# Optimization experiments

Hardware: AMD Instinct MI355X
Metric: run time of the kernel (lower is better)

The kernel has to match this reference:

```python
import jax, jax.numpy as jnp
import numpy as np

D_MODEL = 1024
D_HEAD = 64

def setup_inputs() -> dict:
    key = jax.random.key(0)
    kx, kk, kq, kv = jax.random.split(key, 4)
    s = D_MODEL ** -0.5
    return {
        "x": jax.random.normal(kx, (4, 4096, D_MODEL), dtype=jnp.float32),
        "Wk": jax.random.normal(kk, (D_MODEL, D_HEAD), dtype=jnp.float32) * s,
        "Wq": jax.random.normal(kq, (D_MODEL, D_HEAD), dtype=jnp.float32) * s,
        "Wv": jax.random.normal(kv, (D_MODEL, D_HEAD), dtype=jnp.float32) * s,
    }

def reference(x, Wk, Wq, Wv):
    # x: [B, T, d_model]; Wk/Wq/Wv: [d_model, d_head]
    B, T, _ = x.shape
    d_head = Wk.shape[1]
    k = x @ Wk  # [B, T, d_head]
    q = x @ Wq
    v = x @ Wv
    scores = jnp.einsum("btd,bsd->bts", q, k) * (d_head ** -0.5)  # [B, T, T]
    causal = jnp.tril(jnp.ones((T, T), dtype=bool))
    scores = jnp.where(causal, scores, -jnp.inf)
    weights = jax.nn.softmax(scores, axis=-1)
    return jnp.einsum("bts,bsd->btd", weights, v)
```

## Files before the change

kernel.cpp:

```cpp
#include <hip/hip_runtime.h>

typedef __attribute__((ext_vector_type(8))) short bf16x8;
typedef __attribute__((ext_vector_type(4))) float f32x4;

#define DI __device__ __forceinline__

DI unsigned short f2bf(float f) {
    unsigned int u = __builtin_bit_cast(unsigned int, f);
    u += 0x7fff + ((u >> 16) & 1);
    return (unsigned short)(u >> 16);
}

DI unsigned int cvtpk(float lo, float hi) {
    unsigned int r;
    asm("v_cvt_pk_bf16_f32 %0, %1, %2" : "=v"(r) : "v"(lo), "v"(hi));
    return r;
}

DI void gl_lds16(const void* g, void* l) {
    __builtin_amdgcn_global_load_lds(
        (const __attribute__((address_space(1))) unsigned int*)g,
        (__attribute__((address_space(3))) unsigned int*)l, 16, 0, 0);
}

#define WAITCNT(n) asm volatile("s_waitcnt vmcnt(" #n ")" ::: "memory")

__global__ __launch_bounds__(256) void wt_kernel(
    const float* __restrict__ Wk, const float* __restrict__ Wq,
    const float* __restrict__ Wv, unsigned short* __restrict__ Wt)
{
    __shared__ float ws[64][65];
    const int m = blockIdx.x >> 4, kc = blockIdx.x & 15;
    const float* W = (m == 0) ? Wq : (m == 1) ? Wk : Wv;
    const float scale = (m == 0) ? 0.18033688011112042f : 1.0f;
    const int tid = threadIdx.x;
    #pragma unroll
    for (int r = 0; r < 16; ++r) {
        int idx = r * 256 + tid;
        ws[idx >> 6][idx & 63] = W[(kc * 64 + (idx >> 6)) * 64 + (idx & 63)] * scale;
    }
    __syncthreads();
    const int c = tid >> 2, k4 = (tid & 3) * 16;
    bf16x8 o0, o1;
    #pragma unroll
    for (int j = 0; j < 8; ++j) o0[j] = (short)f2bf(ws[k4 + j][c]);
    #pragma unroll
    for (int j = 0; j < 8; ++j) o1[j] = (short)f2bf(ws[k4 + 8 + j][c]);
    unsigned short* dst = Wt + ((size_t)m * 64 + c) * 1024 + kc * 64 + k4;
    *(bf16x8*)dst = o0;
    *(bf16x8*)(dst + 8) = o1;
}

__global__ __launch_bounds__(256) void proj_kernel(
    const float* __restrict__ x, const unsigned short* __restrict__ Wt,
    unsigned short* __restrict__ qw, unsigned short* __restrict__ kw,
    unsigned short* __restrict__ vT)
{
    __shared__ char LDSx[3][8192];
    __shared__ char LDSb[3][6144];

    const int tid = threadIdx.x;
    const int w = tid >> 6, l = tid & 63;
    const int xr = l & 15, lg = l >> 4;
    const int rb = blockIdx.x & 255, ch = blockIdx.x >> 8;
    const int row0 = rb * 64;

    const char* xsrc = (const char*)x + (size_t)row0 * 4096;
    const char* Wtb = (const char*)Wt;

    const int xrow_l = l >> 3, xcb = (l & 7) * 16;
    const int brow_l = l >> 2, bcb = (l & 3) * 16;

    auto stage = [&](int nb, int s) {
        #pragma unroll
        for (int c = 0; c < 4; ++c) {
            const int ci = w + 4 * c;
            if (ci < 8) {
                const int row = ci * 8 + xrow_l;
                const int sw = (row & 7) << 4;
                gl_lds16(xsrc + (size_t)row * 4096 + (size_t)s * 128 + (xcb ^ sw),
                         LDSx[nb] + ci * 1024);
            } else if (ci < 14) {
                const int c8 = ci - 8;
                const int r = c8 * 16 + brow_l;
                const int sw = ((r >> 1) & 3) << 4;
                const int wtrow = (r >> 5) * 64 + ch * 32 + (r & 31);
                gl_lds16(Wtb + (size_t)wtrow * 2048 + (size_t)s * 64 + (bcb ^ sw),
                         LDSb[nb] + c8 * 1024);
            }
        }
    };

    f32x4 acc[3][2];
    #pragma unroll
    for (int m = 0; m < 3; ++m)
        #pragma unroll
        for (int tt = 0; tt < 2; ++tt) { f32x4 z = {0.f,0.f,0.f,0.f}; acc[m][tt] = z; }

    const int Rw = w * 16 + xr;
    const int swx = (Rw & 7) << 4;

    auto compute = [&](int pb) {
        float4 va = *(const float4*)(LDSx[pb] + Rw * 128 + ((32 * lg) ^ swx));
        float4 vb = *(const float4*)(LDSx[pb] + Rw * 128 + ((32 * lg + 16) ^ swx));
        bf16x8 a;
        a[0] = (short)f2bf(va.x); a[1] = (short)f2bf(va.y);
        a[2] = (short)f2bf(va.z); a[3] = (short)f2bf(va.w);
        a[4] = (short)f2bf(vb.x); a[5] = (short)f2bf(vb.y);
        a[6] = (short)f2bf(vb.z); a[7] = (short)f2bf(vb.w);
        __builtin_amdgcn_s_setprio(1);
        #pragma unroll
        for (int m = 0; m < 3; ++m)
            #pragma unroll
            for (int tt = 0; tt < 2; ++tt) {
                const int rB = m * 32 + tt * 16 + xr;
                bf16x8 bfr = *(const bf16x8*)(LDSb[pb] + rB * 64 +
                                ((16 * lg) ^ (((rB >> 1) & 3) << 4)));
                acc[m][tt] = __builtin_amdgcn_mfma_f32_16x16x32_bf16(a, bfr, acc[m][tt], 0, 0, 0);
            }
        __builtin_amdgcn_s_setprio(0);
    };

    stage(0, 0); stage(1, 1);

    int cb = 0, nb = 2;
    for (int s = 0; s < 32; ++s) {
        if (s == 31) { WAITCNT(0); }
        else if (w < 2) { WAITCNT(4); }
        else { WAITCNT(3); }
        __builtin_amdgcn_sched_barrier(0);
        __builtin_amdgcn_s_barrier();
        if (s + 2 < 32) stage(nb, s + 2);
        compute(cb);
        cb = (cb == 2) ? 0 : cb + 1;
        nb = (nb == 2) ? 0 : nb + 1;
    }

    const int bb = row0 >> 12;
    #pragma unroll
    for (int tt = 0; tt < 2; ++tt) {
        const int col = ch * 32 + tt * 16 + xr;
        unsigned short pv4[4];
        #pragma unroll
        for (int i = 0; i < 4; ++i) {
            const int grow = row0 + w * 16 + 4 * lg + i;
            qw[(size_t)grow * 64 + col] = f2bf(acc[0][tt][i]);
            kw[(size_t)grow * 64 + col] = f2bf(acc[1][tt][i]);
            pv4[i] = f2bf(acc[2][tt][i]);
        }
        const int lr0 = (row0 & 4095) + w * 16 + 4 * lg;
        *(uint2*)&vT[((size_t)bb * 64 + col) * 4096 + lr0] = *(const uint2*)pv4;
    }
}

__global__ __launch_bounds__(256) void attn_kernel(
    const unsigned short* __restrict__ qw, const unsigned short* __restrict__ kw,
    const unsigned short* __restrict__ vT,
    unsigned short* __restrict__ POb, float* __restrict__ Pl)
{
    __shared__ __align__(16) unsigned short Kb[2][4096];
    __shared__ __align__(16) unsigned short Vb[2][4096];
    __shared__ __align__(16) unsigned short Ps[4][16][64];

    const int id = blockIdx.x;
    const int qb = 63 - (id & 63);
    const int b  = (id >> 6) & 3;
    const int c  = id >> 8;
    if (c * 8 > qb) return;

    const int tid = threadIdx.x;
    const int w = tid >> 6, l = tid & 63;
    const int xr = l & 15, g = l >> 4;

    const int t0 = c * 8;
    const int rem0 = qb + 1 - t0;
    const int tcnt = rem0 < 8 ? rem0 : 8;
    const size_t base = (size_t)b * 4096;
    const int qrow = qb * 64 + w * 16;
    const int myrow = qrow + xr;

    bf16x8 aq[2];
    #pragma unroll
    for (int h = 0; h < 2; ++h)
        aq[h] = *(const bf16x8*)(qw + (base + myrow) * 64 + 32 * h + 8 * g);

    const int wo0 = w * 2048, wo1 = wo0 + 1024;
    const int o0 = wo0 + 16 * l, o1 = wo1 + 16 * l;
    const int k0sw = (o0 & ~127) | ((o0 & 127) ^ (((o0 >> 7) & 7) << 4));
    const int k1sw = (o1 & ~127) | ((o1 & 127) ^ (((o1 >> 7) & 7) << 4));
    const size_t v0sw = (size_t)(o0 >> 7) * 8192 + ((o0 & 127) ^ (((o0 >> 7) & 7) << 4));
    const size_t v1sw = (size_t)(o1 >> 7) * 8192 + ((o1 & 127) ^ (((o1 >> 7) & 7) << 4));
    const char* kwb  = (const char*)kw + base * 128;
    const char* vtb0 = (const char*)vT + (size_t)b * 64 * 8192;

    auto stage = [&](int bi, int it) {
        const char* kt = kwb + (size_t)it * 8192;
        gl_lds16(kt + k0sw, (char*)Kb[bi] + wo0);
        gl_lds16(kt + k1sw, (char*)Kb[bi] + wo1);
        const char* vt = vtb0 + (size_t)it * 128;
        gl_lds16(vt + v0sw, (char*)Vb[bi] + wo0);
        gl_lds16(vt + v1sw, (char*)Vb[bi] + wo1);
    };

    f32x4 accO[4];
    #pragma unroll
    for (int t = 0; t < 4; ++t) { f32x4 z = {0.f,0.f,0.f,0.f}; accO[t] = z; }
    float lsum = 0.f;

    const int swz = (xr & 7) << 4;
    char* const psrow = (char*)Ps + w * 2048 + xr * 128;

    stage(0, t0);
    if (tcnt > 1) stage(1, t0 + 1);

    for (int tt = 0; tt < tcnt; ++tt) {
        const int it = t0 + tt;
        const int bi = tt & 1;
        if (tt + 1 < tcnt) { WAITCNT(4); } else { WAITCNT(0); }
        __builtin_amdgcn_sched_barrier(0);
        __builtin_amdgcn_s_barrier();

        const char* kbase = (const char*)Kb[bi];
        f32x4 s[4];
        __builtin_amdgcn_s_setprio(1);
        #pragma unroll
        for (int t = 0; t < 4; ++t) {
            f32x4 z = {0.f,0.f,0.f,0.f};
            s[t] = z;
            #pragma unroll
            for (int h = 0; h < 2; ++h) {
                bf16x8 ak = *(const bf16x8*)(kbase + (xr + 16 * t) * 128 + ((64 * h + 16 * g) ^ swz));
                s[t] = __builtin_amdgcn_mfma_f32_16x16x32_bf16(ak, aq[h], s[t], 0, 0, 0);
            }
        }
        __builtin_amdgcn_s_setprio(0);

        if (it == qb) {
            #pragma unroll
            for (int t = 0; t < 4; ++t)
                #pragma unroll
                for (int i = 0; i < 4; ++i) {
                    const int key = it * 64 + 16 * t + 4 * g + i;
                    if (key > myrow) s[t][i] = -1e30f;
                }
        }

        #pragma unroll
        for (int t = 0; t < 4; ++t)
            #pragma unroll
            for (int i = 0; i < 4; ++i)
                s[t][i] = exp2f(s[t][i]);

        {
            float a0 = (s[0][0] + s[0][1]) + (s[0][2] + s[0][3]);
            float a1 = (s[1][0] + s[1][1]) + (s[1][2] + s[1][3]);
            float a2 = (s[2][0] + s[2][1]) + (s[2][2] + s[2][3]);
            float a3 = (s[3][0] + s[3][1]) + (s[3][2] + s[3][3]);
            lsum += (a0 + a1) + (a2 + a3);
        }

        #pragma unroll
        for (int t = 0; t < 4; ++t) {
            uint2 uu;
            uu.x = cvtpk(s[t][0], s[t][1]);
            uu.y = cvtpk(s[t][2], s[t][3]);
            *(uint2*)(psrow + ((32 * t + 8 * g) ^ swz)) = uu;
        }

        bf16x8 pa[2];
        #pragma unroll
        for (int h = 0; h < 2; ++h)
            pa[h] = *(const bf16x8*)(psrow + ((16 * g + 64 * h) ^ swz));
        const char* vbase = (const char*)Vb[bi];
        __builtin_amdgcn_s_setprio(1);
        #pragma unroll
        for (int t = 0; t < 4; ++t)
            #pragma unroll
            for (int h = 0; h < 2; ++h) {
                bf16x8 av = *(const bf16x8*)(vbase + (16 * t + xr) * 128 + ((64 * h + 16 * g) ^ swz));
                accO[t] = __builtin_amdgcn_mfma_f32_16x16x32_bf16(av, pa[h], accO[t], 0, 0, 0);
            }
        __builtin_amdgcn_s_setprio(0);

        __builtin_amdgcn_s_barrier();
        if (tt + 2 < tcnt) stage(bi, it + 2);
    }

    lsum += __shfl_xor(lsum, 16, 64);
    lsum += __shfl_xor(lsum, 32, 64);

    const size_t prow = (size_t)(b * 8 + c) * 4096 + qrow;
    #pragma unroll
    for (int t = 0; t < 4; ++t) {
        uint2 uu;
        uu.x = cvtpk(accO[t][0], accO[t][1]);
        uu.y = cvtpk(accO[t][2], accO[t][3]);
        *(uint2*)&POb[(prow + xr) * 64 + 16 * t + 4 * g] = uu;
    }
    if (l < 16) Pl[prow + l] = lsum;
}

__global__ __launch_bounds__(256) void merge_kernel(
    const unsigned short* __restrict__ POb, const float* __restrict__ Pl,
    float* __restrict__ out)
{
    const int gid = blockIdx.x * 256 + threadIdx.x;
    const int r = gid >> 2;
    const int c0 = (gid & 3) * 16;
    const int b = r >> 12, lr = r & 4095;
    const int nc = (lr >> 9) + 1;

    float L = 0.f;
    #pragma unroll
    for (int ci = 0; ci < 8; ++ci)
        if (ci < nc) L += Pl[(size_t)(b * 8 + ci) * 4096 + lr];
    const float rL = 1.0f / L;

    float acc[16];
    #pragma unroll
    for (int j = 0; j < 16; ++j) acc[j] = 0.f;

    #pragma unroll
    for (int ci = 0; ci < 8; ++ci) {
        if (ci < nc) {
            const unsigned short* p = POb + ((size_t)(b * 8 + ci) * 4096 + lr) * 64 + c0;
            uint4 u0 = *(const uint4*)p;
            uint4 u1 = *(const uint4*)(p + 8);
            const unsigned int us[8] = {u0.x, u0.y, u0.z, u0.w, u1.x, u1.y, u1.z, u1.w};
            #pragma unroll
            for (int k = 0; k < 8; ++k) {
                acc[2 * k]     += __builtin_bit_cast(float, us[k] << 16);
                acc[2 * k + 1] += __builtin_bit_cast(float, us[k] & 0xFFFF0000u);
            }
        }
    }
    float* op = out + (size_t)r * 64 + c0;
    #pragma unroll
    for (int j = 0; j < 4; ++j) {
        float4 v;
        v.x = acc[4 * j]     * rL;
        v.y = acc[4 * j + 1] * rL;
        v.z = acc[4 * j + 2] * rL;
        v.w = acc[4 * j + 3] * rL;
        *(float4*)(op + 4 * j) = v;
    }
}

extern "C" void kernel_launch(void* const* d_in, const int* in_sizes, int n_in,
                              void* d_out, int out_size, void* d_ws, size_t ws_size,
                              hipStream_t stream) {
    const float* x  = (const float*)d_in[0];
    const float* Wk = (const float*)d_in[1];
    const float* Wq = (const float*)d_in[2];
    const float* Wv = (const float*)d_in[3];
    float* out = (float*)d_out;

    char* wsb = (char*)d_ws;
    unsigned short* POb = (unsigned short*)wsb;
    float* Pl = (float*)(wsb + (size_t)17 * 1024 * 1024);
    unsigned short* Wt = (unsigned short*)(wsb + (size_t)24 * 1024 * 1024);
    unsigned short* qw = Wt + (size_t)3 * 64 * 1024;
    unsigned short* kw = qw + (size_t)16384 * 64;
    unsigned short* vT = kw + (size_t)16384 * 64;

    hipLaunchKernelGGL(wt_kernel, dim3(48), dim3(256), 0, stream, Wk, Wq, Wv, Wt);
    hipLaunchKernelGGL(proj_kernel, dim3(512), dim3(256), 0, stream, x, Wt, qw, kw, vT);
    hipLaunchKernelGGL(attn_kernel, dim3(2048), dim3(256), 0, stream, qw, kw, vT, POb, Pl);
    hipLaunchKernelGGL(merge_kernel, dim3(256), dim3(256), 0, stream, POb, Pl, out);
}
```

Measured before the change: 64.89 us.

## Split attention waves over query-row pairs and key halves for fragment reuse

Each wave now handles 32 query rows against half of the 64-key tile, instead of 16 rows against all keys. Every K and V fragment read from LDS then feeds two MFMAs, so LDS read traffic per MFMA is halved. The two key-half partial outputs and row sums are reduced at the end through LDS scratch reusing the K/V buffers. The cost is extra accumulator registers, two extra block barriers and an LDS reduction in the epilogue.

```diff
diff --git a/kernel.cpp b/kernel.cpp
--- a/kernel.cpp
+++ b/kernel.cpp
@@ -160,7 +160,7 @@
 {
     __shared__ __align__(16) unsigned short Kb[2][4096];
     __shared__ __align__(16) unsigned short Vb[2][4096];
-    __shared__ __align__(16) unsigned short Ps[4][16][64];
+    __shared__ __align__(16) unsigned short Ps[4][2][16][32];
 
     const int id = blockIdx.x;
     const int qb = 63 - (id & 63);
@@ -171,18 +171,23 @@
     const int tid = threadIdx.x;
     const int w = tid >> 6, l = tid & 63;
     const int xr = l & 15, g = l >> 4;
+    const int rw = w >> 1;
+    const int kw2 = w & 1;
 
     const int t0 = c * 8;
     const int rem0 = qb + 1 - t0;
     const int tcnt = rem0 < 8 ? rem0 : 8;
     const size_t base = (size_t)b * 4096;
-    const int qrow = qb * 64 + w * 16;
-    const int myrow = qrow + xr;
-
-    bf16x8 aq[2];
-    #pragma unroll
-    for (int h = 0; h < 2; ++h)
-        aq[h] = *(const bf16x8*)(qw + (base + myrow) * 64 + 32 * h + 8 * g);
+    const int qrow0 = qb * 64 + rw * 32;
+    const int myrowA = qrow0 + xr;
+    const int myrowB = qrow0 + 16 + xr;
+
+    bf16x8 aqA[2], aqB[2];
+    #pragma unroll
+    for (int h = 0; h < 2; ++h) {
+        aqA[h] = *(const bf16x8*)(qw + (base + myrowA) * 64 + 32 * h + 8 * g);
+        aqB[h] = *(const bf16x8*)(qw + (base + myrowB) * 64 + 32 * h + 8 * g);
+    }
 
     const int wo0 = w * 2048, wo1 = wo0 + 1024;
     const int o0 = wo0 + 16 * l, o1 = wo1 + 16 * l;
@@ -202,13 +207,17 @@
         gl_lds16(vt + v1sw, (char*)Vb[bi] + wo1);
     };
 
-    f32x4 accO[4];
-    #pragma unroll
-    for (int t = 0; t < 4; ++t) { f32x4 z = {0.f,0.f,0.f,0.f}; accO[t] = z; }
-    float lsum = 0.f;
+    f32x4 accO[2][4];
+    #pragma unroll
+    for (int gr = 0; gr < 2; ++gr)
+        #pragma unroll
+        for (int t = 0; t < 4; ++t) { f32x4 z = {0.f,0.f,0.f,0.f}; accO[gr][t] = z; }
+    float lsA = 0.f, lsB = 0.f;
 
     const int swz = (xr & 7) << 4;
-    char* const psrow = (char*)Ps + w * 2048 + xr * 128;
+    const int swzP = (xr & 3) << 4;
+    char* const psrowA = (char*)Ps + w * 2048 + xr * 64;
+    char* const psrowB = psrowA + 1024;
 
     stage(0, t0);
     if (tcnt > 1) stage(1, t0 + 1);
@@ -220,84 +229,105 @@
         __builtin_amdgcn_sched_barrier(0);
         __builtin_amdgcn_s_barrier();
 
-        const char* kbase = (const char*)Kb[bi];
-        f32x4 s[4];
+        const char* kbase = (const char*)Kb[bi] + kw2 * 4096;
+        f32x4 sA[2], sB[2];
         __builtin_amdgcn_s_setprio(1);
         #pragma unroll
-        for (int t = 0; t < 4; ++t) {
+        for (int t = 0; t < 2; ++t) {
             f32x4 z = {0.f,0.f,0.f,0.f};
-            s[t] = z;
+            sA[t] = z; sB[t] = z;
             #pragma unroll
             for (int h = 0; h < 2; ++h) {
-                bf16x8 ak = *(const bf16x8*)(kbase + (xr + 16 * t) * 128 + ((64 * h + 16 * g) ^ swz));
-                s[t] = __builtin_amdgcn_mfma_f32_16x16x32_bf16(ak, aq[h], s[t], 0, 0, 0);
+                bf16x8 ak = *(const bf16x8*)(kbase + (16 * t + xr) * 128 + ((64 * h + 16 * g) ^ swz));
+                sA[t] = __builtin_amdgcn_mfma_f32_16x16x32_bf16(ak, aqA[h], sA[t], 0, 0, 0);
+                sB[t] = __builtin_amdgcn_mfma_f32_16x16x32_bf16(ak, aqB[h], sB[t], 0, 0, 0);
             }
         }
         __builtin_amdgcn_s_setprio(0);
 
         if (it == qb) {
             #pragma unroll
-            for (int t = 0; t < 4; ++t)
+            for (int t = 0; t < 2; ++t)
                 #pragma unroll
                 for (int i = 0; i < 4; ++i) {
-                    const int key = it * 64 + 16 * t + 4 * g + i;
-                    if (key > myrow) s[t][i] = -1e30f;
+                    const int key = it * 64 + kw2 * 32 + 16 * t + 4 * g + i;
+                    if (key > myrowA) sA[t][i] = -1e30f;
+                    if (key > myrowB) sB[t][i] = -1e30f;
                 }
         }
 
         #pragma unroll
-        for (int t = 0; t < 4; ++t)
-            #pragma unroll
-            for (int i = 0; i < 4; ++i)
-                s[t][i] = exp2f(s[t][i]);
-
-        {
-            float a0 = (s[0][0] + s[0][1]) + (s[0][2] + s[0][3]);
-            float a1 = (s[1][0] + s[1][1]) + (s[1][2] + s[1][3]);
-            float a2 = (s[2][0] + s[2][1]) + (s[2][2] + s[2][3]);
-            float a3 = (s[3][0] + s[3][1]) + (s[3][2] + s[3][3]);
-            lsum += (a0 + a1) + (a2 + a3);
-        }
-
-        #pragma unroll
-        for (int t = 0; t < 4; ++t) {
-            uint2 uu;
-            uu.x = cvtpk(s[t][0], s[t][1]);
-            uu.y = cvtpk(s[t][2], s[t][3]);
-            *(uint2*)(psrow + ((32 * t + 8 * g) ^ swz)) = uu;
-        }
-
-        bf16x8 pa[2];
-        #pragma unroll
-        for (int h = 0; h < 2; ++h)
-            pa[h] = *(const bf16x8*)(psrow + ((16 * g + 64 * h) ^ swz));
+        for (int t = 0; t < 2; ++t)
+            #pragma unroll
+            for (int i = 0; i < 4; ++i) {
+                sA[t][i] = exp2f(sA[t][i]);
+                sB[t][i] = exp2f(sB[t][i]);
+            }
+        lsA += ((sA[0][0] + sA[0][1]) + (sA[0][2] + sA[0][3]))
+             + ((sA[1][0] + sA[1][1]) + (sA[1][2] + sA[1][3]));
+        lsB += ((sB[0][0] + sB[0][1]) + (sB[0][2] + sB[0][3]))
+             + ((sB[1][0] + sB[1][1]) + (sB[1][2] + sB[1][3]));
+
+        #pragma unroll
+        for (int t = 0; t < 2; ++t) {
+            uint2 uA, uB;
+            uA.x = cvtpk(sA[t][0], sA[t][1]); uA.y = cvtpk(sA[t][2], sA[t][3]);
+            uB.x = cvtpk(sB[t][0], sB[t][1]); uB.y = cvtpk(sB[t][2], sB[t][3]);
+            *(uint2*)(psrowA + ((32 * t + 8 * g) ^ swzP)) = uA;
+            *(uint2*)(psrowB + ((32 * t + 8 * g) ^ swzP)) = uB;
+        }
+        bf16x8 paA = *(const bf16x8*)(psrowA + ((16 * g) ^ swzP));
+        bf16x8 paB = *(const bf16x8*)(psrowB + ((16 * g) ^ swzP));
+
         const char* vbase = (const char*)Vb[bi];
         __builtin_amdgcn_s_setprio(1);
         #pragma unroll
-        for (int t = 0; t < 4; ++t)
-            #pragma unroll
-            for (int h = 0; h < 2; ++h) {
-                bf16x8 av = *(const bf16x8*)(vbase + (16 * t + xr) * 128 + ((64 * h + 16 * g) ^ swz));
-                accO[t] = __builtin_amdgcn_mfma_f32_16x16x32_bf16(av, pa[h], accO[t], 0, 0, 0);
-            }
+        for (int t = 0; t < 4; ++t) {
+            bf16x8 av = *(const bf16x8*)(vbase + (16 * t + xr) * 128 + ((kw2 * 64 + 16 * g) ^ swz));
+            accO[0][t] = __builtin_amdgcn_mfma_f32_16x16x32_bf16(av, paA, accO[0][t], 0, 0, 0);
+            accO[1][t] = __builtin_amdgcn_mfma_f32_16x16x32_bf16(av, paB, accO[1][t], 0, 0, 0);
+        }
         __builtin_amdgcn_s_setprio(0);
 
         __builtin_amdgcn_s_barrier();
         if (tt + 2 < tcnt) stage(bi, it + 2);
     }
 
-    lsum += __shfl_xor(lsum, 16, 64);
-    lsum += __shfl_xor(lsum, 32, 64);
-
-    const size_t prow = (size_t)(b * 8 + c) * 4096 + qrow;
-    #pragma unroll
-    for (int t = 0; t < 4; ++t) {
-        uint2 uu;
-        uu.x = cvtpk(accO[t][0], accO[t][1]);
-        uu.y = cvtpk(accO[t][2], accO[t][3]);
-        *(uint2*)&POb[(prow + xr) * 64 + 16 * t + 4 * g] = uu;
-    }
-    if (l < 16) Pl[prow + l] = lsum;
+    lsA += __shfl_xor(lsA, 16, 64); lsA += __shfl_xor(lsA, 32, 64);
+    lsB += __shfl_xor(lsB, 16, 64); lsB += __shfl_xor(lsB, 32, 64);
+
+    __syncthreads();
+    float* scr  = (float*)Kb;
+    float* scrL = (float*)Vb;
+    if (kw2) {
+        #pragma unroll
+        for (int gr = 0; gr < 2; ++gr)
+            #pragma unroll
+            for (int t = 0; t < 4; ++t)
+                *(f32x4*)(scr + rw * 2048 + (gr * 4 + t) * 256 + g * 64 + xr * 4) = accO[gr][t];
+        if (l < 16) {
+            scrL[rw * 128 + l] = lsA;
+            scrL[rw * 128 + 16 + l] = lsB;
+        }
+    }
+    __syncthreads();
+    if (!kw2) {
+        const size_t prow = (size_t)(b * 8 + c) * 4096 + qb * 64 + rw * 32;
+        #pragma unroll
+        for (int gr = 0; gr < 2; ++gr)
+            #pragma unroll
+            for (int t = 0; t < 4; ++t) {
+                f32x4 o = accO[gr][t] + *(const f32x4*)(scr + rw * 2048 + (gr * 4 + t) * 256 + g * 64 + xr * 4);
+                uint2 uu;
+                uu.x = cvtpk(o[0], o[1]);
+                uu.y = cvtpk(o[2], o[3]);
+                *(uint2*)&POb[(prow + gr * 16 + xr) * 64 + 16 * t + 4 * g] = uu;
+            }
+        if (l < 16) {
+            Pl[prow + l]      = lsA + scrL[rw * 128 + l];
+            Pl[prow + 16 + l] = lsB + scrL[rw * 128 + 16 + l];
+        }
+    }
 }
 
 __global__ __launch_bounds__(256) void merge_kernel(
```

Measured after the change: 67.31 us. +3.7%, slower.

## Prepack weights in MFMA fragment order and give each projection block all columns

Applied to the files above, without the earlier changes.

The weight-transpose kernel now writes W in MFMA B-fragment order, one contiguous 12 KB chunk per K-step, so the projection kernel can load B tiles with linear copies and no swizzle math. Each projection block now covers 32 rows and all 64 output columns, with waves split by row group and column half, instead of 64 rows by 32 columns. Each x element is therefore read from global memory once rather than twice, at the cost of reading more weight bytes per block. Wait counts become uniform across waves.

```diff
diff --git a/kernel.cpp b/kernel.cpp
--- a/kernel.cpp
+++ b/kernel.cpp
@@ -27,68 +27,54 @@
 
 __global__ __launch_bounds__(256) void wt_kernel(
     const float* __restrict__ Wk, const float* __restrict__ Wq,
-    const float* __restrict__ Wv, unsigned short* __restrict__ Wt)
+    const float* __restrict__ Wv, unsigned short* __restrict__ Wtf)
 {
-    __shared__ float ws[64][65];
-    const int m = blockIdx.x >> 4, kc = blockIdx.x & 15;
-    const float* W = (m == 0) ? Wq : (m == 1) ? Wk : Wv;
-    const float scale = (m == 0) ? 0.18033688011112042f : 1.0f;
+    const int s = blockIdx.x;
     const int tid = threadIdx.x;
-    #pragma unroll
-    for (int r = 0; r < 16; ++r) {
-        int idx = r * 256 + tid;
-        ws[idx >> 6][idx & 63] = W[(kc * 64 + (idx >> 6)) * 64 + (idx & 63)] * scale;
-    }
-    __syncthreads();
-    const int c = tid >> 2, k4 = (tid & 3) * 16;
-    bf16x8 o0, o1;
-    #pragma unroll
-    for (int j = 0; j < 8; ++j) o0[j] = (short)f2bf(ws[k4 + j][c]);
-    #pragma unroll
-    for (int j = 0; j < 8; ++j) o1[j] = (short)f2bf(ws[k4 + 8 + j][c]);
-    unsigned short* dst = Wt + ((size_t)m * 64 + c) * 1024 + kc * 64 + k4;
-    *(bf16x8*)dst = o0;
-    *(bf16x8*)(dst + 8) = o1;
+    const int chalf = tid >> 7, t = (tid >> 6) & 1, lane = tid & 63;
+    const int col = chalf * 32 + t * 16 + (lane & 15);
+    const int k0 = s * 32 + (lane >> 4) * 8;
+
+    const float* Wm[3] = {Wq, Wk, Wv};
+    #pragma unroll
+    for (int m = 0; m < 3; ++m) {
+        const float scale = (m == 0) ? 0.18033688011112042f : 1.0f;
+        const float* W = Wm[m];
+        bf16x8 o;
+        #pragma unroll
+        for (int j = 0; j < 8; ++j)
+            o[j] = (short)f2bf(W[(size_t)(k0 + j) * 64 + col] * scale);
+        *(bf16x8*)(Wtf + ((((size_t)s * 3 + m) * 4) + chalf * 2 + t) * 1024 / 2 + lane * 8) = o;
+    }
 }
 
 __global__ __launch_bounds__(256) void proj_kernel(
-    const float* __restrict__ x, const unsigned short* __restrict__ Wt,
+    const float* __restrict__ x, const unsigned short* __restrict__ Wtf,
     unsigned short* __restrict__ qw, unsigned short* __restrict__ kw,
     unsigned short* __restrict__ vT)
 {
-    __shared__ char LDSx[3][8192];
-    __shared__ char LDSb[3][6144];
+    __shared__ char LDSx[3][4096];
+    __shared__ char LDSb[3][12288];
 
     const int tid = threadIdx.x;
     const int w = tid >> 6, l = tid & 63;
     const int xr = l & 15, lg = l >> 4;
-    const int rb = blockIdx.x & 255, ch = blockIdx.x >> 8;
-    const int row0 = rb * 64;
+    const int rgrp = w >> 1, chalf = w & 1;
+    const int row0 = blockIdx.x * 32;
 
     const char* xsrc = (const char*)x + (size_t)row0 * 4096;
-    const char* Wtb = (const char*)Wt;
-
-    const int xrow_l = l >> 3, xcb = (l & 7) * 16;
-    const int brow_l = l >> 2, bcb = (l & 3) * 16;
+    const char* Wtb = (const char*)Wtf;
+
+    const int srow = w * 8 + (l >> 3);
+    const int ssl = (l & 7) * 16;
 
     auto stage = [&](int nb, int s) {
-        #pragma unroll
-        for (int c = 0; c < 4; ++c) {
-            const int ci = w + 4 * c;
-            if (ci < 8) {
-                const int row = ci * 8 + xrow_l;
-                const int sw = (row & 7) << 4;
-                gl_lds16(xsrc + (size_t)row * 4096 + (size_t)s * 128 + (xcb ^ sw),
-                         LDSx[nb] + ci * 1024);
-            } else if (ci < 14) {
-                const int c8 = ci - 8;
-                const int r = c8 * 16 + brow_l;
-                const int sw = ((r >> 1) & 3) << 4;
-                const int wtrow = (r >> 5) * 64 + ch * 32 + (r & 31);
-                gl_lds16(Wtb + (size_t)wtrow * 2048 + (size_t)s * 64 + (bcb ^ sw),
-                         LDSb[nb] + c8 * 1024);
-            }
-        }
+        gl_lds16(xsrc + (size_t)srow * 4096 + s * 128 + (ssl ^ ((srow & 7) << 4)),
+                 LDSx[nb] + w * 1024);
+        const char* wsrc = Wtb + (size_t)s * 12288;
+        gl_lds16(wsrc + (w)      * 1024 + l * 16, LDSb[nb] + (w)      * 1024);
+        gl_lds16(wsrc + (4 + w)  * 1024 + l * 16, LDSb[nb] + (4 + w)  * 1024);
+        gl_lds16(wsrc + (8 + w)  * 1024 + l * 16, LDSb[nb] + (8 + w)  * 1024);
     };
 
     f32x4 acc[3][2];
@@ -97,7 +83,7 @@
         #pragma unroll
         for (int tt = 0; tt < 2; ++tt) { f32x4 z = {0.f,0.f,0.f,0.f}; acc[m][tt] = z; }
 
-    const int Rw = w * 16 + xr;
+    const int Rw = rgrp * 16 + xr;
     const int swx = (Rw & 7) << 4;
 
     auto compute = [&](int pb) {
@@ -113,9 +99,8 @@
         for (int m = 0; m < 3; ++m)
             #pragma unroll
             for (int tt = 0; tt < 2; ++tt) {
-                const int rB = m * 32 + tt * 16 + xr;
-                bf16x8 bfr = *(const bf16x8*)(LDSb[pb] + rB * 64 +
-                                ((16 * lg) ^ (((rB >> 1) & 3) << 4)));
+                bf16x8 bfr = *(const bf16x8*)(LDSb[pb] +
+                                (m * 4 + chalf * 2 + tt) * 1024 + l * 16);
                 acc[m][tt] = __builtin_amdgcn_mfma_f32_16x16x32_bf16(a, bfr, acc[m][tt], 0, 0, 0);
             }
         __builtin_amdgcn_s_setprio(0);
@@ -125,9 +110,7 @@
 
     int cb = 0, nb = 2;
     for (int s = 0; s < 32; ++s) {
-        if (s == 31) { WAITCNT(0); }
-        else if (w < 2) { WAITCNT(4); }
-        else { WAITCNT(3); }
+        if (s == 31) { WAITCNT(0); } else { WAITCNT(4); }
         __builtin_amdgcn_sched_barrier(0);
         __builtin_amdgcn_s_barrier();
         if (s + 2 < 32) stage(nb, s + 2);
@@ -139,16 +122,16 @@
     const int bb = row0 >> 12;
     #pragma unroll
     for (int tt = 0; tt < 2; ++tt) {
-        const int col = ch * 32 + tt * 16 + xr;
+        const int col = chalf * 32 + tt * 16 + xr;
         unsigned short pv4[4];
         #pragma unroll
         for (int i = 0; i < 4; ++i) {
-            const int grow = row0 + w * 16 + 4 * lg + i;
+            const int grow = row0 + rgrp * 16 + 4 * lg + i;
             qw[(size_t)grow * 64 + col] = f2bf(acc[0][tt][i]);
             kw[(size_t)grow * 64 + col] = f2bf(acc[1][tt][i]);
             pv4[i] = f2bf(acc[2][tt][i]);
         }
-        const int lr0 = (row0 & 4095) + w * 16 + 4 * lg;
+        const int lr0 = (row0 & 4095) + rgrp * 16 + 4 * lg;
         *(uint2*)&vT[((size_t)bb * 64 + col) * 4096 + lr0] = *(const uint2*)pv4;
     }
 }
@@ -358,13 +341,13 @@
     char* wsb = (char*)d_ws;
     unsigned short* POb = (unsigned short*)wsb;
     float* Pl = (float*)(wsb + (size_t)17 * 1024 * 1024);
-    unsigned short* Wt = (unsigned short*)(wsb + (size_t)24 * 1024 * 1024);
-    unsigned short* qw = Wt + (size_t)3 * 64 * 1024;
+    unsigned short* Wtf = (unsigned short*)(wsb + (size_t)24 * 1024 * 1024);
+    unsigned short* qw = Wtf + (size_t)3 * 64 * 1024;
     unsigned short* kw = qw + (size_t)16384 * 64;
     unsigned short* vT = kw + (size_t)16384 * 64;
 
-    hipLaunchKernelGGL(wt_kernel, dim3(48), dim3(256), 0, stream, Wk, Wq, Wv, Wt);
-    hipLaunchKernelGGL(proj_kernel, dim3(512), dim3(256), 0, stream, x, Wt, qw, kw, vT);
+    hipLaunchKernelGGL(wt_kernel, dim3(32), dim3(256), 0, stream, Wk, Wq, Wv, Wtf);
+    hipLaunchKernelGGL(proj_kernel, dim3(512), dim3(256), 0, stream, x, Wtf, qw, kw, vT);
     hipLaunchKernelGGL(attn_kernel, dim3(2048), dim3(256), 0, stream, qw, kw, vT, POb, Pl);
     hipLaunchKernelGGL(merge_kernel, dim3(256), dim3(256), 0, stream, POb, Pl, out);
 }
```

New measurement: 69.78 us. +7.5%, slower.
